# Kernel optimization log

Hardware: AMD Instinct MI355X
Metric: run time of the kernel (lower is better)

The kernel has to match this reference:

```python
import jax, jax.numpy as jnp
import numpy as np

B, S, D = 32, 64, 16
OUT_F = 8
IN_DIM = S * D                      # 1024
N_QUAD = (IN_DIM + IN_DIM ** 2) // 2  # 524800 upper-triangular (incl. diag) entries
OUT_DIM = OUT_F * S                 # 512

# Static upper-triangular indices (row-major, includes diagonal) — same order as
# torch.triu_indices(in_dim, in_dim).
_TRIU_R, _TRIU_C = np.triu_indices(IN_DIM)


def setup_inputs() -> dict:
    key = jax.random.key(0)
    k1, k2, k3 = jax.random.split(key, 3)
    input_ = jax.random.normal(k1, (B, S, D), dtype=jnp.float32)
    in_total = IN_DIM + N_QUAD
    bound = 1.0 / np.sqrt(in_total)
    W = jax.random.uniform(k2, (OUT_DIM, in_total), dtype=jnp.float32, minval=-bound, maxval=bound)
    b = jax.random.uniform(k3, (OUT_DIM,), dtype=jnp.float32, minval=-bound, maxval=bound)
    return {"input_": input_, "W": W, "b": b}


def reference(input_, W, b):
    Bsz = input_.shape[0]
    x_flat = input_.reshape(Bsz, IN_DIM)                     # [B, in_dim]
    r = jnp.asarray(_TRIU_R)
    c = jnp.asarray(_TRIU_C)
    # Quadratic features: upper-triangular entries of outer(x, x) without
    # materializing the full [B, in_dim, in_dim] outer product.
    x_squared = x_flat[:, r] * x_flat[:, c]                  # [B, N_QUAD]
    x = jnp.concatenate([x_flat, x_squared], axis=-1)        # [B, in_dim + N_QUAD]
    out = x @ W.T + b                                        # [B, out_f * S]
    return out.reshape(Bsz, S, OUT_F)
```

## Files before the change

### kernel.cpp

```cpp
#include <hip/hip_runtime.h>
#include <hip/hip_bf16.h>

#define B_SZ     32
#define IN_DIM   1024
#define K_TOTAL  525824
#define OUT_DIM  512
#define NCH      4108
#define KGN      128
#define F_BYTES  ((size_t)NCH * 8192)
#define P_ELEMS  ((size_t)KGN * B_SZ * OUT_DIM)
#define NEED_WS  (F_BYTES + P_ELEMS * 4)

typedef __attribute__((ext_vector_type(8))) short bfrag;
typedef __attribute__((ext_vector_type(4))) float f32x4;

#define GLD16(g, l) __builtin_amdgcn_global_load_lds(                      \
    (const __attribute__((address_space(1))) void*)(g),                    \
    (__attribute__((address_space(3))) void*)(l), 16, 0, 0)

__device__ inline unsigned bf16r(float f)
{
    unsigned u = __builtin_bit_cast(unsigned, f);
    return (u + 0x7FFFu + ((u >> 16) & 1u)) >> 16;
}
__device__ inline unsigned pk2(float a, float b)
{
    return bf16r(a) | (bf16r(b) << 16);
}

__global__ void bias_init_kernel(const float* __restrict__ bias, float* __restrict__ out)
{
    int i = blockIdx.x * 256 + threadIdx.x;
    out[i] = bias[i & (OUT_DIM - 1)];
}

__global__ __launch_bounds__(256)
void feat_pack_kernel(const float* __restrict__ x, int4* __restrict__ fp)
{
    const int chunk = blockIdx.x;
    const int tid   = threadIdx.x;

    #pragma unroll
    for (int i = 0; i < 2; ++i) {
        const int unit = tid + i * 256;
        const int kb   = unit >> 5;
        const int b    = unit & 31;
        const int k0   = chunk * 128 + kb * 8;
        const float* xb = x + b * IN_DIM;

        float v[8];
        if (chunk < 8) {
            #pragma unroll
            for (int e = 0; e < 8; ++e) v[e] = xb[k0 + e];
        } else {
            int t = k0 - IN_DIM;
            float disc = 4198401.0f - 8.0f * (float)t;
            int r = (int)((2049.0f - sqrtf(disc)) * 0.5f);
            int off = r * IN_DIM - ((r * (r - 1)) >> 1);
            if (t < off) { --r; off = r * IN_DIM - ((r * (r - 1)) >> 1); }
            else if (t >= off + (IN_DIM - r)) { off += IN_DIM - r; ++r; }
            int c_ = r + (t - off);
            #pragma unroll
            for (int e = 0; e < 8; ++e) {
                v[e] = xb[r] * xb[c_];
                if (c_ == IN_DIM - 1) { ++r; c_ = r; } else { ++c_; }
            }
        }
        int4 pk;
        pk.x = (int)pk2(v[0], v[1]);
        pk.y = (int)pk2(v[2], v[3]);
        pk.z = (int)pk2(v[4], v[5]);
        pk.w = (int)pk2(v[6], v[7]);
        fp[(size_t)chunk * 512 + unit] = pk;
    }
}

__global__ __launch_bounds__(256, 4)
void qgemm_mfma_kernel(const int4* __restrict__ fp,
                       const float* __restrict__ W,
                       float* __restrict__ partial)
{
    __shared__ int4 fbuf[3][512];

    const int tid  = threadIdx.x;
    const int lane = tid & 63;
    const int wv_  = tid >> 6;
    const int lrow = lane & 15;
    const int lkb  = lane >> 4;

    const int og = blockIdx.x >> 7;
    const int kg = blockIdx.x & (KGN - 1);

    const int o_base = og * 64 + wv_ * 16;
    const float* wlane = W + (size_t)(o_base + lrow) * K_TOTAL;
    const char*  fpB   = (const char*)fp + (size_t)lane * 16;

    f32x4 acc0 = {0.f, 0.f, 0.f, 0.f};
    f32x4 acc1 = {0.f, 0.f, 0.f, 0.f};
    float4 wc[8], wn[8];

    #define WLOADR(dst, cc)                                                     \
    do {                                                                        \
        const float* wp_ = wlane + (size_t)(cc) * 128 + lkb * 8;                \
        _Pragma("unroll")                                                       \
        for (int q_ = 0; q_ < 4; ++q_) {                                        \
            dst[2*q_]   = *(const float4*)(wp_ + q_ * 32);                      \
            dst[2*q_+1] = *(const float4*)(wp_ + q_ * 32 + 4);                  \
        }                                                                       \
    } while (0)

    #define STAGEF(s, cc)                                                       \
    do {                                                                        \
        const char* gp_ = fpB + (size_t)(cc) * 8192;                            \
        GLD16(gp_ + wv_ * 1024,        (char*)&fbuf[s][0] + wv_ * 1024);        \
        GLD16(gp_ + 4096 + wv_ * 1024, (char*)&fbuf[s][0] + 4096 + wv_ * 1024); \
    } while (0)

    #define COMPUTE(cbuf)                                                       \
    do {                                                                        \
        const int4* bp_ = &fbuf[cbuf][0];                                       \
        _Pragma("unroll")                                                       \
        for (int q_ = 0; q_ < 4; ++q_) {                                        \
            int4 tw_;                                                           \
            tw_.x = (int)pk2(wc[2*q_].x,   wc[2*q_].y);                         \
            tw_.y = (int)pk2(wc[2*q_].z,   wc[2*q_].w);                         \
            tw_.z = (int)pk2(wc[2*q_+1].x, wc[2*q_+1].y);                       \
            tw_.w = (int)pk2(wc[2*q_+1].z, wc[2*q_+1].w);                       \
            const bfrag bw_ = __builtin_bit_cast(bfrag, tw_);                   \
            const int ub_ = (q_ * 4 + lkb) * 32 + lrow;                         \
            const bfrag a0_ = __builtin_bit_cast(bfrag, bp_[ub_]);              \
            const bfrag a1_ = __builtin_bit_cast(bfrag, bp_[ub_ + 16]);         \
            acc0 = __builtin_amdgcn_mfma_f32_16x16x32_bf16(a0_, bw_, acc0, 0, 0, 0); \
            acc1 = __builtin_amdgcn_mfma_f32_16x16x32_bf16(a1_, bw_, acc1, 0, 0, 0); \
        }                                                                       \
    } while (0)

    int c = kg;
    STAGEF(0, c);
    WLOADR(wn, c);
    STAGEF(1, c + KGN);

    int cb = 0, sb = 2;
    for (; c < NCH; c += KGN) {
        asm volatile("s_waitcnt vmcnt(2)" ::: "memory");
        __builtin_amdgcn_s_barrier();
        #pragma unroll
        for (int j = 0; j < 8; ++j) wc[j] = wn[j];
        const int cw = (c + KGN     < NCH) ? c + KGN     : c;
        const int cf = (c + 2 * KGN < NCH) ? c + 2 * KGN : c;
        WLOADR(wn, cw);
        STAGEF(sb, cf);
        COMPUTE(cb);
        cb = (cb == 2) ? 0 : cb + 1;
        sb = (sb == 2) ? 0 : sb + 1;
    }
    asm volatile("s_waitcnt vmcnt(0)" ::: "memory");

    #undef COMPUTE
    #undef STAGEF
    #undef WLOADR

    float* pb = partial + (size_t)kg * (B_SZ * OUT_DIM) + o_base + lrow;
    const int r0 = lkb * 4;
    #pragma unroll
    for (int r = 0; r < 4; ++r) {
        pb[(size_t)(r0 + r) * OUT_DIM]      = acc0[r];
        pb[(size_t)(16 + r0 + r) * OUT_DIM] = acc1[r];
    }
}

__global__ __launch_bounds__(256)
void reduce_kernel(const float* __restrict__ partial,
                   const float* __restrict__ bias,
                   float* __restrict__ out)
{
    const int idx = blockIdx.x * 256 + threadIdx.x;
    float s = bias[idx & (OUT_DIM - 1)];
    const float* p = partial + idx;
    #pragma unroll 8
    for (int kg = 0; kg < KGN; ++kg)
        s += p[(size_t)kg * (B_SZ * OUT_DIM)];
    out[idx] = s;
}

__global__ __launch_bounds__(512, 2)
void qgemm_fallback_kernel(const float* __restrict__ x,
                           const float* __restrict__ W,
                           float* __restrict__ out)
{
    __shared__ float xt[B_SZ][512];

    const int tid  = threadIdx.x;
    const int lane = tid & 63;
    const int wave = tid >> 6;
    const int bgrp = wave & 3;
    const int ogrp = wave >> 2;

    const int og  = blockIdx.x & 31;
    const int kgf = blockIdx.x >> 5;

    const int o_base = og * 16 + ogrp * 8;
    const int b_base = bgrp * 8;

    float acc[8][8];
    #pragma unroll
    for (int i = 0; i < 8; ++i)
        #pragma unroll
        for (int o = 0; o < 8; ++o) acc[i][o] = 0.f;

    const int nch = (K_TOTAL + 511) / 512;
    for (int chunk = kgf; chunk < nch; chunk += 16) {
        const int k = chunk * 512 + tid;
        __syncthreads();
        if (k < IN_DIM) {
            #pragma unroll
            for (int b = 0; b < B_SZ; ++b)
                xt[b][tid] = x[b * IN_DIM + k];
        } else {
            const int t = k - IN_DIM;
            double disc = 4198401.0 - 8.0 * (double)t;
            int r = (int)((2049.0 - sqrt(disc)) * 0.5);
            int off = r * IN_DIM - ((r * (r - 1)) >> 1);
            if (t < off) { --r; off = r * IN_DIM - ((r * (r - 1)) >> 1); }
            else if (t >= off + (IN_DIM - r)) { off += IN_DIM - r; ++r; }
            const int ccol = r + (t - off);
            #pragma unroll
            for (int b = 0; b < B_SZ; ++b)
                xt[b][tid] = x[b * IN_DIM + r] * x[b * IN_DIM + ccol];
        }
        __syncthreads();

        const float* wrow = W + (size_t)o_base * K_TOTAL + (size_t)chunk * 512;
        #pragma unroll
        for (int pass = 0; pass < 2; ++pass) {
            const int kk = pass * 256 + lane * 4;
            float4 wv[8];
            #pragma unroll
            for (int o = 0; o < 8; ++o)
                wv[o] = *(const float4*)(wrow + (size_t)o * K_TOTAL + kk);
            float4 xv[8];
            #pragma unroll
            for (int i = 0; i < 8; ++i)
                xv[i] = *(const float4*)&xt[b_base + i][kk];
            #pragma unroll
            for (int o = 0; o < 8; ++o)
                #pragma unroll
                for (int i = 0; i < 8; ++i)
                    acc[i][o] += xv[i].x * wv[o].x + xv[i].y * wv[o].y
                               + xv[i].z * wv[o].z + xv[i].w * wv[o].w;
        }
    }

    #pragma unroll
    for (int i = 0; i < 8; ++i)
        #pragma unroll
        for (int o = 0; o < 8; ++o) {
            float v = acc[i][o];
            #pragma unroll
            for (int m = 1; m < 64; m <<= 1)
                v += __shfl_xor(v, m);
            acc[i][o] = v;
        }

    if (lane == 0) {
        #pragma unroll
        for (int i = 0; i < 8; ++i)
            #pragma unroll
            for (int o = 0; o < 8; ++o)
                atomicAdd(&out[(b_base + i) * OUT_DIM + o_base + o], acc[i][o]);
    }
}

extern "C" void kernel_launch(void* const* d_in, const int* in_sizes, int n_in,
                              void* d_out, int out_size, void* d_ws, size_t ws_size,
                              hipStream_t stream)
{
    const float* x    = (const float*)d_in[0];
    const float* W    = (const float*)d_in[1];
    const float* bias = (const float*)d_in[2];
    float* out = (float*)d_out;

    if (ws_size >= NEED_WS) {
        int4*  fpk  = (int4*)d_ws;
        float* part = (float*)((char*)d_ws + F_BYTES);
        hipLaunchKernelGGL(feat_pack_kernel, dim3(NCH), dim3(256), 0, stream, x, fpk);
        hipLaunchKernelGGL(qgemm_mfma_kernel, dim3(8 * KGN), dim3(256), 0, stream,
                           fpk, W, part);
        hipLaunchKernelGGL(reduce_kernel, dim3(64), dim3(256), 0, stream,
                           part, bias, out);
    } else {
        hipLaunchKernelGGL(bias_init_kernel, dim3(64), dim3(256), 0, stream, bias, out);
        hipLaunchKernelGGL(qgemm_fallback_kernel, dim3(512), dim3(512), 0, stream,
                           x, W, out);
    }
}
```

Baseline: 313.0 us.

## Process chunk pairs per iteration with larger stages and early weight conversion

```diff
diff --git a/kernel.cpp b/kernel.cpp
--- a/kernel.cpp
+++ b/kernel.cpp
@@ -6,6 +6,7 @@
 #define K_TOTAL  525824
 #define OUT_DIM  512
 #define NCH      4108
+#define NPAIR    2054
 #define KGN      128
 #define F_BYTES  ((size_t)NCH * 8192)
 #define P_ELEMS  ((size_t)KGN * B_SZ * OUT_DIM)
@@ -75,12 +76,12 @@
     }
 }
 
-__global__ __launch_bounds__(256, 4)
+__global__ __launch_bounds__(256, 2)
 void qgemm_mfma_kernel(const int4* __restrict__ fp,
                        const float* __restrict__ W,
                        float* __restrict__ partial)
 {
-    __shared__ int4 fbuf[3][512];
+    __shared__ int4 fbuf[3][1024];
 
     const int tid  = threadIdx.x;
     const int lane = tid & 63;
@@ -97,68 +98,88 @@
 
     f32x4 acc0 = {0.f, 0.f, 0.f, 0.f};
     f32x4 acc1 = {0.f, 0.f, 0.f, 0.f};
-    float4 wc[8], wn[8];
-
-    #define WLOADR(dst, cc)                                                     \
+    float4 wn[16];
+    int4   wcb[8];
+
+    #define WLOADP(pp)                                                          \
     do {                                                                        \
-        const float* wp_ = wlane + (size_t)(cc) * 128 + lkb * 8;                \
+        const float* wp_ = wlane + (size_t)(pp) * 256 + lkb * 8;                \
         _Pragma("unroll")                                                       \
         for (int q_ = 0; q_ < 4; ++q_) {                                        \
-            dst[2*q_]   = *(const float4*)(wp_ + q_ * 32);                      \
-            dst[2*q_+1] = *(const float4*)(wp_ + q_ * 32 + 4);                  \
+            wn[2*q_]   = *(const float4*)(wp_ + q_ * 32);                       \
+            wn[2*q_+1] = *(const float4*)(wp_ + q_ * 32 + 4);                   \
+        }                                                                       \
+        _Pragma("unroll")                                                       \
+        for (int q_ = 0; q_ < 4; ++q_) {                                        \
+            wn[8+2*q_]   = *(const float4*)(wp_ + 128 + q_ * 32);               \
+            wn[8+2*q_+1] = *(const float4*)(wp_ + 128 + q_ * 32 + 4);           \
         }                                                                       \
     } while (0)
 
-    #define STAGEF(s, cc)                                                       \
+    #define STAGEF(s, pp)                                                       \
     do {                                                                        \
-        const char* gp_ = fpB + (size_t)(cc) * 8192;                            \
-        GLD16(gp_ + wv_ * 1024,        (char*)&fbuf[s][0] + wv_ * 1024);        \
-        GLD16(gp_ + 4096 + wv_ * 1024, (char*)&fbuf[s][0] + 4096 + wv_ * 1024); \
+        const char* gp_ = fpB + (size_t)(pp) * 16384 + wv_ * 4096;              \
+        _Pragma("unroll")                                                       \
+        for (int j_ = 0; j_ < 4; ++j_)                                          \
+            GLD16(gp_ + j_ * 1024, (char*)&fbuf[s][0] + wv_ * 4096 + j_ * 1024);\
+    } while (0)
+
+    #define CVTW()                                                              \
+    do {                                                                        \
+        _Pragma("unroll")                                                       \
+        for (int e_ = 0; e_ < 8; ++e_) {                                        \
+            int4 tw_;                                                           \
+            tw_.x = (int)pk2(wn[2*e_].x,   wn[2*e_].y);                         \
+            tw_.y = (int)pk2(wn[2*e_].z,   wn[2*e_].w);                         \
+            tw_.z = (int)pk2(wn[2*e_+1].x, wn[2*e_+1].y);                       \
+            tw_.w = (int)pk2(wn[2*e_+1].z, wn[2*e_+1].w);                       \
+            wcb[e_] = tw_;                                                      \
+        }                                                                       \
     } while (0)
 
     #define COMPUTE(cbuf)                                                       \
     do {                                                                        \
         const int4* bp_ = &fbuf[cbuf][0];                                       \
         _Pragma("unroll")                                                       \
-        for (int q_ = 0; q_ < 4; ++q_) {                                        \
-            int4 tw_;                                                           \
-            tw_.x = (int)pk2(wc[2*q_].x,   wc[2*q_].y);                         \
-            tw_.y = (int)pk2(wc[2*q_].z,   wc[2*q_].w);                         \
-            tw_.z = (int)pk2(wc[2*q_+1].x, wc[2*q_+1].y);                       \
-            tw_.w = (int)pk2(wc[2*q_+1].z, wc[2*q_+1].w);                       \
-            const bfrag bw_ = __builtin_bit_cast(bfrag, tw_);                   \
-            const int ub_ = (q_ * 4 + lkb) * 32 + lrow;                         \
-            const bfrag a0_ = __builtin_bit_cast(bfrag, bp_[ub_]);              \
-            const bfrag a1_ = __builtin_bit_cast(bfrag, bp_[ub_ + 16]);         \
-            acc0 = __builtin_amdgcn_mfma_f32_16x16x32_bf16(a0_, bw_, acc0, 0, 0, 0); \
-            acc1 = __builtin_amdgcn_mfma_f32_16x16x32_bf16(a1_, bw_, acc1, 0, 0, 0); \
-        }                                                                       \
+        for (int s_ = 0; s_ < 2; ++s_)                                          \
+            _Pragma("unroll")                                                   \
+            for (int q_ = 0; q_ < 4; ++q_) {                                    \
+                const bfrag bw_ = __builtin_bit_cast(bfrag, wcb[s_*4 + q_]);    \
+                const int ub_ = s_ * 512 + (q_ * 4 + lkb) * 32 + lrow;          \
+                const bfrag a0_ = __builtin_bit_cast(bfrag, bp_[ub_]);          \
+                const bfrag a1_ = __builtin_bit_cast(bfrag, bp_[ub_ + 16]);     \
+                acc0 = __builtin_amdgcn_mfma_f32_16x16x32_bf16(a0_, bw_, acc0, 0, 0, 0); \
+                acc1 = __builtin_amdgcn_mfma_f32_16x16x32_bf16(a1_, bw_, acc1, 0, 0, 0); \
+            }                                                                   \
     } while (0)
 
-    int c = kg;
-    STAGEF(0, c);
-    WLOADR(wn, c);
-    STAGEF(1, c + KGN);
+    const int n  = 16 + (kg < 6 ? 1 : 0);
+    int pc = kg;
+
+    STAGEF(0, pc);
+    WLOADP(pc);
+    STAGEF(1, pc + KGN);
 
     int cb = 0, sb = 2;
-    for (; c < NCH; c += KGN) {
-        asm volatile("s_waitcnt vmcnt(2)" ::: "memory");
+    for (int t = 0; t < n; ++t) {
+        asm volatile("s_waitcnt vmcnt(4)" ::: "memory");
         __builtin_amdgcn_s_barrier();
-        #pragma unroll
-        for (int j = 0; j < 8; ++j) wc[j] = wn[j];
-        const int cw = (c + KGN     < NCH) ? c + KGN     : c;
-        const int cf = (c + 2 * KGN < NCH) ? c + 2 * KGN : c;
-        WLOADR(wn, cw);
-        STAGEF(sb, cf);
+        CVTW();
+        const int pw = (t + 1 < n) ? pc + KGN     : pc;
+        const int pf = (t + 2 < n) ? pc + 2 * KGN : pw;
+        WLOADP(pw);
+        STAGEF(sb, pf);
         COMPUTE(cb);
         cb = (cb == 2) ? 0 : cb + 1;
         sb = (sb == 2) ? 0 : sb + 1;
+        pc += KGN;
     }
     asm volatile("s_waitcnt vmcnt(0)" ::: "memory");
 
     #undef COMPUTE
+    #undef CVTW
     #undef STAGEF
-    #undef WLOADR
+    #undef WLOADP
 
     float* pb = partial + (size_t)kg * (B_SZ * OUT_DIM) + o_base + lrow;
     const int r0 = lkb * 4;
```

After: 282.2 us. -9.8%, faster.

## Stage W tiles through swizzled LDS via async global_load_lds double buffering

Applied to the files above, without the earlier changes.

```diff
diff --git a/kernel.cpp b/kernel.cpp
--- a/kernel.cpp
+++ b/kernel.cpp
@@ -75,12 +75,13 @@
     }
 }
 
-__global__ __launch_bounds__(256, 4)
+__global__ __launch_bounds__(256, 2)
 void qgemm_mfma_kernel(const int4* __restrict__ fp,
                        const float* __restrict__ W,
                        float* __restrict__ partial)
 {
-    __shared__ int4 fbuf[3][512];
+    __shared__ int4 wlds[2][64][32];
+    __shared__ int4 fbuf[2][512];
 
     const int tid  = threadIdx.x;
     const int lane = tid & 63;
@@ -91,74 +92,80 @@
     const int og = blockIdx.x >> 7;
     const int kg = blockIdx.x & (KGN - 1);
 
-    const int o_base = og * 64 + wv_ * 16;
-    const float* wlane = W + (size_t)(o_base + lrow) * K_TOTAL;
-    const char*  fpB   = (const char*)fp + (size_t)lane * 16;
+    const int o_blk  = og * 64;
+    const int o_base = o_blk + wv_ * 16;
 
     f32x4 acc0 = {0.f, 0.f, 0.f, 0.f};
     f32x4 acc1 = {0.f, 0.f, 0.f, 0.f};
-    float4 wc[8], wn[8];
-
-    #define WLOADR(dst, cc)                                                     \
+
+    #define WSTAGE(s, cc)                                                       \
     do {                                                                        \
-        const float* wp_ = wlane + (size_t)(cc) * 128 + lkb * 8;                \
+        _Pragma("unroll")                                                       \
+        for (int j_ = 0; j_ < 8; ++j_) {                                        \
+            const int rl_ = 2 * j_ + (lane >> 5);                               \
+            const char* src_ = (const char*)(W                                  \
+                + (size_t)(o_blk + wv_ * 16 + rl_) * K_TOTAL                    \
+                + (size_t)(cc) * 128)                                           \
+                + (((lane & 31) << 4) ^ ((rl_ & 7) << 4));                      \
+            GLD16(src_, (char*)&wlds[s][wv_ * 16 + 2 * j_][0]);                 \
+        }                                                                       \
+    } while (0)
+
+    #define FSTAGE(s, cc)                                                       \
+    do {                                                                        \
+        const char* gp_ = (const char*)fp + (size_t)(cc) * 8192                 \
+                        + wv_ * 2048 + (size_t)(lane << 4);                     \
+        GLD16(gp_,        (char*)&fbuf[s][0] + wv_ * 2048);                     \
+        GLD16(gp_ + 1024, (char*)&fbuf[s][0] + wv_ * 2048 + 1024);              \
+    } while (0)
+
+    #define COMPUTE(s)                                                          \
+    do {                                                                        \
+        const int r_  = wv_ * 16 + lrow;                                        \
+        const int s7_ = lrow & 7;                                               \
         _Pragma("unroll")                                                       \
         for (int q_ = 0; q_ < 4; ++q_) {                                        \
-            dst[2*q_]   = *(const float4*)(wp_ + q_ * 32);                      \
-            dst[2*q_+1] = *(const float4*)(wp_ + q_ * 32 + 4);                  \
-        }                                                                       \
-    } while (0)
-
-    #define STAGEF(s, cc)                                                       \
-    do {                                                                        \
-        const char* gp_ = fpB + (size_t)(cc) * 8192;                            \
-        GLD16(gp_ + wv_ * 1024,        (char*)&fbuf[s][0] + wv_ * 1024);        \
-        GLD16(gp_ + 4096 + wv_ * 1024, (char*)&fbuf[s][0] + 4096 + wv_ * 1024); \
-    } while (0)
-
-    #define COMPUTE(cbuf)                                                       \
-    do {                                                                        \
-        const int4* bp_ = &fbuf[cbuf][0];                                       \
-        _Pragma("unroll")                                                       \
-        for (int q_ = 0; q_ < 4; ++q_) {                                        \
+            const int sl_ = lkb * 2 + q_ * 8;                                   \
+            const float4 f0_ = __builtin_bit_cast(float4, wlds[s][r_][sl_ ^ s7_]);       \
+            const float4 f1_ = __builtin_bit_cast(float4, wlds[s][r_][(sl_ + 1) ^ s7_]); \
             int4 tw_;                                                           \
-            tw_.x = (int)pk2(wc[2*q_].x,   wc[2*q_].y);                         \
-            tw_.y = (int)pk2(wc[2*q_].z,   wc[2*q_].w);                         \
-            tw_.z = (int)pk2(wc[2*q_+1].x, wc[2*q_+1].y);                       \
-            tw_.w = (int)pk2(wc[2*q_+1].z, wc[2*q_+1].w);                       \
+            tw_.x = (int)pk2(f0_.x, f0_.y);                                     \
+            tw_.y = (int)pk2(f0_.z, f0_.w);                                     \
+            tw_.z = (int)pk2(f1_.x, f1_.y);                                     \
+            tw_.w = (int)pk2(f1_.z, f1_.w);                                     \
             const bfrag bw_ = __builtin_bit_cast(bfrag, tw_);                   \
             const int ub_ = (q_ * 4 + lkb) * 32 + lrow;                         \
-            const bfrag a0_ = __builtin_bit_cast(bfrag, bp_[ub_]);              \
-            const bfrag a1_ = __builtin_bit_cast(bfrag, bp_[ub_ + 16]);         \
+            const bfrag a0_ = __builtin_bit_cast(bfrag, fbuf[s][ub_]);          \
+            const bfrag a1_ = __builtin_bit_cast(bfrag, fbuf[s][ub_ + 16]);     \
             acc0 = __builtin_amdgcn_mfma_f32_16x16x32_bf16(a0_, bw_, acc0, 0, 0, 0); \
             acc1 = __builtin_amdgcn_mfma_f32_16x16x32_bf16(a1_, bw_, acc1, 0, 0, 0); \
         }                                                                       \
     } while (0)
 
+    const int n = (kg < 12) ? 33 : 32;
     int c = kg;
-    STAGEF(0, c);
-    WLOADR(wn, c);
-    STAGEF(1, c + KGN);
-
-    int cb = 0, sb = 2;
-    for (; c < NCH; c += KGN) {
-        asm volatile("s_waitcnt vmcnt(2)" ::: "memory");
+
+    WSTAGE(0, c);       FSTAGE(0, c);
+    WSTAGE(1, c + KGN); FSTAGE(1, c + KGN);
+
+    for (int t = 0; t < n; ++t) {
+        if (t < n - 1)
+            asm volatile("s_waitcnt vmcnt(10)" ::: "memory");
+        else
+            asm volatile("s_waitcnt vmcnt(0)" ::: "memory");
         __builtin_amdgcn_s_barrier();
-        #pragma unroll
-        for (int j = 0; j < 8; ++j) wc[j] = wn[j];
-        const int cw = (c + KGN     < NCH) ? c + KGN     : c;
-        const int cf = (c + 2 * KGN < NCH) ? c + 2 * KGN : c;
-        WLOADR(wn, cw);
-        STAGEF(sb, cf);
-        COMPUTE(cb);
-        cb = (cb == 2) ? 0 : cb + 1;
-        sb = (sb == 2) ? 0 : sb + 1;
-    }
-    asm volatile("s_waitcnt vmcnt(0)" ::: "memory");
+        COMPUTE(t & 1);
+        __builtin_amdgcn_s_barrier();
+        if (t + 2 < n) {
+            WSTAGE(t & 1, c + 2 * KGN);
+            FSTAGE(t & 1, c + 2 * KGN);
+        }
+        c += KGN;
+    }
 
     #undef COMPUTE
-    #undef STAGEF
-    #undef WLOADR
+    #undef FSTAGE
+    #undef WSTAGE
 
     float* pb = partial + (size_t)kg * (B_SZ * OUT_DIM) + o_base + lrow;
     const int r0 = lkb * 4;
```

Result: faster. 280.5 us (-10.4%).
